# Kernel tuning notes

Measured on AMD Instinct MI355X. Metric: run time of the kernel, lower is better.

Reference implementation:

```python
import jax, jax.numpy as jnp
import numpy as np
from jax import lax

L, B, T_IMG, T_TXT = 12, 2, 256, 64
E, H, G = 1024, 16, 2730
V = 16416  # image_vocab_count + 1
C = E // H
EPS = 1e-6  # flax LayerNorm default


def _ln(x, scale, bias):
    mu = jnp.mean(x, -1, keepdims=True)
    var = jnp.var(x, -1, keepdims=True)
    y = (x - mu) * lax.rsqrt(var + EPS)
    if scale is not None:
        y = y * scale
    if bias is not None:
        y = y + bias
    return y


def _attend(k, v, q, mask, o_w):
    # k,v: [B,K,H,C]  q: [B,Q,H,C]  mask: [B,K]
    bias = jnp.where(mask, 0.0, -jnp.inf)[:, None, None, :]
    w = jnp.einsum('bqhc,bkhc->bhqk', q, k) + bias
    w = jax.nn.softmax(w, axis=-1)
    out = jnp.einsum('bhqk,bkhc->bqhc', w, v)
    return out.reshape(out.shape[0], out.shape[1], E) @ o_w


def setup_inputs():
    key = jax.random.key(0)
    ks = jax.random.split(key, 16)
    s = 0.02
    n = lambda k, shape: jax.random.normal(k, shape, jnp.float32) * s
    return dict(
        encoder_state=n(ks[0], (B, T_TXT, E)),
        keys_state=jnp.zeros((L, B, T_IMG, H, C), jnp.float32),
        values_state=jnp.zeros((L, B, T_IMG, H, C), jnp.float32),
        attention_mask=jnp.ones((B, T_TXT), jnp.bool_),
        prev_token=5000,
        token_index=100,
        embed_tok=n(ks[1], (V, E)),
        embed_pos=n(ks[2], (T_IMG, E)),
        ln_emb_s=jnp.ones((E,), jnp.float32),
        ln_emb_b=jnp.zeros((E,), jnp.float32),
        final_ln_b=jnp.zeros((E,), jnp.float32),
        lm_head_w=n(ks[3], (E, V)),
        pre_sa_ln_b=jnp.zeros((L, E), jnp.float32),
        sa_q_w=n(ks[4], (L, E, E)), sa_k_w=n(ks[5], (L, E, E)),
        sa_v_w=n(ks[6], (L, E, E)), sa_o_w=n(ks[7], (L, E, E)),
        sa_ln_s=jnp.ones((L, E), jnp.float32), sa_ln_b=jnp.zeros((L, E), jnp.float32),
        pre_ca_ln_b=jnp.zeros((L, E), jnp.float32),
        ca_q_w=n(ks[8], (L, E, E)), ca_k_w=n(ks[9], (L, E, E)),
        ca_v_w=n(ks[10], (L, E, E)), ca_o_w=n(ks[11], (L, E, E)),
        ca_ln_s=jnp.ones((L, E), jnp.float32), ca_ln_b=jnp.zeros((L, E), jnp.float32),
        glu_ln0_b=jnp.zeros((L, E), jnp.float32),
        glu_fc0_w=n(ks[12], (L, E, G)), glu_fc1_w=n(ks[13], (L, E, G)),
        glu_ln1_b=jnp.zeros((L, G), jnp.float32),
        glu_fc2_w=n(ks[14], (L, G, E)),
    )


def _decode_step(encoder_state, keys_state, values_state, attention_mask,
                 prev_token, token_index, embed_tok, embed_pos,
                 ln_emb_s, ln_emb_b, final_ln_b, lm_head_w, layer_params):
    ones = jnp.ones((B, 1), jnp.int32)
    ds = embed_tok[prev_token * ones] + embed_pos[token_index * ones]  # [B,1,E]
    ds = _ln(ds, ln_emb_s, ln_emb_b)
    self_mask = jnp.broadcast_to(jnp.arange(T_IMG) < token_index + 1, (B, T_IMG))
    scale = C ** 0.5

    def step(ds, xs):
        ks_l, vs_l, p = xs  # per-layer KV cache [B,T_IMG,H,C] and params
        (pre_sa_b, qw, kw, vw, ow, sa_s, sa_b,
         pre_ca_b, cqw, ckw, cvw, cow, ca_s, ca_b,
         g0b, f0, f1, g1b, f2) = p
        # --- self attention with KV-cache append ---
        residual = ds
        x = _ln(ds, None, pre_sa_b)
        ks_l = lax.dynamic_update_slice(ks_l, (x @ kw).reshape(B, 1, H, C), (0, token_index, 0, 0))
        vs_l = lax.dynamic_update_slice(vs_l, (x @ vw).reshape(B, 1, H, C), (0, token_index, 0, 0))
        q = (x @ qw).reshape(B, 1, H, C) / scale
        x = _attend(ks_l, vs_l, q, self_mask, ow)
        ds = residual + _ln(x, sa_s, sa_b)
        # --- cross attention over encoder state ---
        residual = ds
        x = _ln(ds, None, pre_ca_b)
        ek = (encoder_state @ ckw).reshape(B, T_TXT, H, C)
        ev = (encoder_state @ cvw).reshape(B, T_TXT, H, C)
        q = (x @ cqw).reshape(B, 1, H, C) / scale
        x = _attend(ek, ev, q, attention_mask, cow)
        ds = residual + _ln(x, ca_s, ca_b)
        # --- GLU FFN ---
        residual = ds
        z = _ln(ds, None, g0b)
        w = jax.nn.gelu(z @ f0, approximate=False)
        z = _ln(w * (z @ f1), None, g1b)
        ds = residual + z @ f2
        return ds, (ks_l, vs_l)

    ds, (keys_state, values_state) = lax.scan(step, ds, (keys_state, values_state, layer_params))
    ds = _ln(ds, None, final_ln_b)
    logits = ds @ lm_head_w  # [B,1,V]
    return logits, keys_state, values_state


def reference(encoder_state, keys_state, values_state, attention_mask, prev_token,
              token_index, embed_tok, embed_pos, ln_emb_s, ln_emb_b, final_ln_b,
              lm_head_w, pre_sa_ln_b, sa_q_w, sa_k_w, sa_v_w, sa_o_w, sa_ln_s,
              sa_ln_b, pre_ca_ln_b, ca_q_w, ca_k_w, ca_v_w, ca_o_w, ca_ln_s,
              ca_ln_b, glu_ln0_b, glu_fc0_w, glu_fc1_w, glu_ln1_b, glu_fc2_w):
    layer_params = (pre_sa_ln_b, sa_q_w, sa_k_w, sa_v_w, sa_o_w, sa_ln_s, sa_ln_b,
                    pre_ca_ln_b, ca_q_w, ca_k_w, ca_v_w, ca_o_w, ca_ln_s, ca_ln_b,
                    glu_ln0_b, glu_fc0_w, glu_fc1_w, glu_ln1_b, glu_fc2_w)
    return _decode_step(encoder_state, keys_state, values_state, attention_mask,
                        prev_token, token_index, embed_tok, embed_pos,
                        ln_emb_s, ln_emb_b, final_ln_b, lm_head_w, layer_params)
```

## Files before the change

### kernel.cpp

```cpp
#include <hip/hip_runtime.h>
#include <math.h>

#define LAYERS 12
#define EE 1024
#define GG 2730
#define VV 16416
#define EPS 1e-6f

#define OFF_EK 0
#define OFF_EV 1572864
#define OFF_DS 3145728
#define NSLOT 37
#define OFF_ACC (OFF_DS + NSLOT*2048)
#define ACC_STRIDE 28672
#define AQ 0
#define AK 2048
#define AV 4096
#define AY 6144
#define AQC 8192
#define AY2 10240
#define AA 12288
#define AB2 17748
#define ACC_TOTAL (LAYERS*ACC_STRIDE)
#define ZERO_FLOATS (NSLOT*2048 + ACC_TOTAL)

#define KVL 524288
#define KVB 262144

struct MegaP {
  const float* enc; const float* keys_in; const float* values_in;
  const int* maski; const int* pt; const int* ti;
  const float* tok; const float* pos; const float* ln_s; const float* ln_b;
  const float* final_b; const float* lm_w;
  const float* pre_sa_b; const float* saq; const float* sak; const float* sav;
  const float* sao; const float* sas; const float* sab;
  const float* pre_ca_b; const float* caq; const float* ckw; const float* cvw;
  const float* cao; const float* cas; const float* cab;
  const float* g0b; const float* f0; const float* f1; const float* g1b; const float* f2;
  float* logits; float* keys_out; float* values_out; float* ws;
};

__device__ __forceinline__ void red4(float* sm, float& a, float& b, float& c, float& d){
  #pragma unroll
  for(int o=32;o;o>>=1){ a+=__shfl_down(a,o); b+=__shfl_down(b,o); c+=__shfl_down(c,o); d+=__shfl_down(d,o); }
  int w=threadIdx.x>>6, l=threadIdx.x&63;
  __syncthreads();
  if(l==0){ sm[w]=a; sm[4+w]=b; sm[8+w]=c; sm[12+w]=d; }
  __syncthreads();
  a=sm[0]+sm[1]+sm[2]+sm[3]; b=sm[4]+sm[5]+sm[6]+sm[7];
  c=sm[8]+sm[9]+sm[10]+sm[11]; d=sm[12]+sm[13]+sm[14]+sm[15];
}

__device__ __forceinline__ void ln_stats_g(const float* v, int K, float* sm,
    float& mu0, float& rs0, float& mu1, float& rs1){
  float s0=0,q0=0,s1=0,q1=0;
  for(int i=threadIdx.x;i<K;i+=256){ float a=v[i], b=v[K+i]; s0+=a;q0+=a*a;s1+=b;q1+=b*b; }
  red4(sm,s0,q0,s1,q1);
  mu0=s0/K; mu1=s1/K;
  rs0=rsqrtf(fmaxf(q0/K-mu0*mu0,0.f)+EPS);
  rs1=rsqrtf(fmaxf(q1/K-mu1*mu1,0.f)+EPS);
}

__device__ __forceinline__ void ln_stats_l(float (*Ds)[1024], float* sm,
    float& mu0, float& rs0, float& mu1, float& rs1){
  float s0=0,q0=0,s1=0,q1=0;
  for(int i=threadIdx.x;i<EE;i+=256){ float a=Ds[0][i], b=Ds[1][i]; s0+=a;q0+=a*a;s1+=b;q1+=b*b; }
  red4(sm,s0,q0,s1,q1);
  mu0=s0/EE; mu1=s1/EE;
  rs0=rsqrtf(fmaxf(q0/EE-mu0*mu0,0.f)+EPS);
  rs1=rsqrtf(fmaxf(q1/EE-mu1*mu1,0.f)+EPS);
}

__device__ __forceinline__ void build_ds3(const float* dsi, const float* accL,
    const float* sasl, const float* sabl, const float* casl, const float* cabl,
    float (*Ds)[1024], float* sm){
  float mu0,rs0,mu1,rs1;
  ln_stats_g(accL+AY, EE, sm, mu0,rs0,mu1,rs1);
  for(int i=threadIdx.x;i<EE;i+=256){ float sc=sasl[i], bi=sabl[i];
    Ds[0][i]=dsi[i]    + (accL[AY+i]-mu0)*rs0*sc + bi;
    Ds[1][i]=dsi[EE+i] + (accL[AY+EE+i]-mu1)*rs1*sc + bi; }
  ln_stats_g(accL+AY2, EE, sm, mu0,rs0,mu1,rs1);
  for(int i=threadIdx.x;i<EE;i+=256){ float sc=casl[i], bi=cabl[i];
    Ds[0][i] += (accL[AY2+i]-mu0)*rs0*sc + bi;
    Ds[1][i] += (accL[AY2+EE+i]-mu1)*rs1*sc + bi; }
}

__global__ __launch_bounds__(256)
void k_init(MegaP p){
  __shared__ float As[128][33];
  __shared__ float Bs[32][33];
  const int t=threadIdx.x, bid=blockIdx.x;
  if (bid < 768){
    int lp = bid>>5, cx = bid&31;
    int l = lp>>1, proj = lp&1;
    const float* Wt = (proj? p.cvw : p.ckw) + (size_t)l*EE*EE;
    float* outp = p.ws + (proj? OFF_EV : OFF_EK) + (size_t)l*128*EE;
    int c0 = cx*32;
    int tx=t&7, ty=t>>3;
    float acc[4][4];
    #pragma unroll
    for(int i=0;i<4;i++){ acc[i][0]=0;acc[i][1]=0;acc[i][2]=0;acc[i][3]=0; }
    float ar[16], br[4];
    #pragma unroll
    for(int j=0;j<16;j++){ int i=t+j*256; ar[j]=p.enc[(size_t)(i>>5)*EE + (i&31)]; }
    #pragma unroll
    for(int j=0;j<4;j++){ int i=t+j*256; br[j]=Wt[(size_t)(i>>5)*EE + c0 + (i&31)]; }
    for (int it=0; it<32; ++it){
      #pragma unroll
      for(int j=0;j<16;j++){ int i=t+j*256; As[i>>5][i&31]=ar[j]; }
      #pragma unroll
      for(int j=0;j<4;j++){ int i=t+j*256; Bs[i>>5][i&31]=br[j]; }
      __syncthreads();
      if (it<31){
        int k0n=(it+1)*32;
        #pragma unroll
        for(int j=0;j<16;j++){ int i=t+j*256; ar[j]=p.enc[(size_t)(i>>5)*EE + k0n + (i&31)]; }
        #pragma unroll
        for(int j=0;j<4;j++){ int i=t+j*256; br[j]=Wt[(size_t)((i>>5)+k0n)*EE + c0 + (i&31)]; }
      }
      #pragma unroll
      for (int k=0;k<32;k++){
        float b0=Bs[k][tx*4+0], b1=Bs[k][tx*4+1], b2=Bs[k][tx*4+2], b3=Bs[k][tx*4+3];
        #pragma unroll
        for (int rr=0;rr<4;rr++){
          float av = As[ty+32*rr][k];
          acc[rr][0]+=av*b0; acc[rr][1]+=av*b1; acc[rr][2]+=av*b2; acc[rr][3]+=av*b3;
        }
      }
      __syncthreads();
    }
    #pragma unroll
    for (int rr=0;rr<4;rr++)
      #pragma unroll
      for (int j=0;j<4;j++)
        outp[(size_t)(ty+32*rr)*EE + c0 + tx*4+j] = acc[rr][j];
  } else {
    float* ev = &As[0][0];
    float* smv = &Bs[0][0];
    int ptv = p.pt[0], tiv = p.ti[0];
    float s0=0,q0=0,d1=0,d2=0;
    for(int i=t;i<EE;i+=256){ float v=p.tok[(size_t)ptv*EE+i]+p.pos[(size_t)tiv*EE+i]; ev[i]=v; s0+=v; q0+=v*v; }
    red4(smv,s0,q0,d1,d2);
    float mu=s0/EE, rs=rsqrtf(fmaxf(q0/EE-mu*mu,0.f)+EPS);
    float* ds0 = p.ws + OFF_DS;
    __syncthreads();
    for(int i=t;i<EE;i+=256){ float y=(ev[i]-mu)*rs*p.ln_s[i]+p.ln_b[i]; ds0[i]=y; ds0[EE+i]=y; }
  }
}

__global__ __launch_bounds__(256)
void k_qkv(MegaP p, int l){
  __shared__ float Xs[2][1024];
  __shared__ float sm[16];
  const int t=threadIdx.x;
  const float* dsi = p.ws + OFF_DS + (size_t)(3*l)*2048;
  float* accL = p.ws + OFF_ACC + (size_t)l*ACC_STRIDE;
  const size_t lE2=(size_t)l*EE*EE, lE=(size_t)l*EE;
  float mu0,rs0,mu1,rs1;
  ln_stats_g(dsi, EE, sm, mu0,rs0,mu1,rs1);
  for(int i=t;i<EE;i+=256){ float bi=p.pre_sa_b[lE+i];
    Xs[0][i]=(dsi[i]-mu0)*rs0+bi; Xs[1][i]=(dsi[EE+i]-mu1)*rs1+bi; }
  __syncthreads();
  int c = blockIdx.x*256 + t;
  int sel = c>>10, cc = c&1023;
  const float* W = (sel==0? p.saq : sel==1? p.sak : p.sav) + lE2;
  float* O = accL + (sel==0? AQ : sel==1? AK : AV);
  int k0 = blockIdx.y*16;
  const float* wp = W + (size_t)k0*EE + cc;
  float a0=0,a1=0;
  #pragma unroll
  for(int k=0;k<16;k++){ float w=*wp; wp+=EE; a0+=Xs[0][k0+k]*w; a1+=Xs[1][k0+k]*w; }
  atomicAdd(&O[cc],a0); atomicAdd(&O[EE+cc],a1);
}

__global__ __launch_bounds__(256)
void k_selfo(MegaP p, int l){
  __shared__ float Ds[2][1024];
  __shared__ float att[2][256];
  __shared__ float sm[16];
  const int t=threadIdx.x, bkid=blockIdx.x, tiv=p.ti[0];
  float* accL = p.ws + OFF_ACC + (size_t)l*ACC_STRIDE;
  const size_t lE2=(size_t)l*EE*EE;
  int cg=bkid&3, h=(bkid>>2)&15, sub=(bkid>>6)&3, hoff=h*64;
  if (t < 128){ int bb2=t>>6, c2=t&63; Ds[bb2][c2] = accL[AQ + bb2*EE + hoff + c2]*0.125f; }
  __syncthreads();
  for(int bb2=0;bb2<2;bb2++)
    for(int tt=t; tt<=tiv; tt+=256){
      const float* kr = (tt<tiv) ? (p.keys_in + (size_t)l*KVL + (size_t)bb2*KVB + (size_t)tt*EE + hoff)
                                 : (accL + AK + bb2*EE + hoff);
      float d=0;
      #pragma unroll
      for(int c2=0;c2<64;c2++) d += Ds[bb2][c2]*kr[c2];
      att[bb2][tt] = d;
    }
  __syncthreads();
  int wv=t>>6, l2=t&63;
  if (wv<2){
    float m=-3.4e38f;
    for(int tt=l2; tt<=tiv; tt+=64) m=fmaxf(m, att[wv][tt]);
    #pragma unroll
    for(int o=32;o;o>>=1) m=fmaxf(m,__shfl_xor(m,o));
    float s=0;
    for(int tt=l2; tt<=tiv; tt+=64){ float e=__expf(att[wv][tt]-m); att[wv][tt]=e; s+=e; }
    #pragma unroll
    for(int o=32;o;o>>=1) s+=__shfl_xor(s,o);
    if(l2==0) sm[8+wv]=1.f/s;
  }
  __syncthreads();
  {
    int bb2=t>>7, j=(t>>3)&15, part=t&7, colh=sub*16+j;
    float v=0;
    for(int tt=part; tt<=tiv; tt+=8){
      float vv = (tt<tiv)? p.values_in[(size_t)l*KVL + (size_t)bb2*KVB + (size_t)tt*EE + hoff + colh]
                         : accL[AV + bb2*EE + hoff + colh];
      v += att[bb2][tt]*vv;
    }
    v += __shfl_down(v,4,8); v += __shfl_down(v,2,8); v += __shfl_down(v,1,8);
    if(part==0) Ds[bb2][512+j] = v*sm[8+bb2];
  }
  __syncthreads();
  {
    int c = cg*256+t, kb = hoff + sub*16;
    const float* wp = p.sao + lE2 + (size_t)kb*EE + c;
    float a0=0,a1=0;
    #pragma unroll
    for(int j2=0;j2<16;j2++){ float w=wp[(size_t)j2*EE]; a0+=Ds[0][512+j2]*w; a1+=Ds[1][512+j2]*w; }
    atomicAdd(&accL[AY+c],a0); atomicAdd(&accL[AY+EE+c],a1);
  }
  if (cg==0 && sub==0){
    int bb2=t>>7, kv=(t>>6)&1, c2=t&63;
    float val = accL[(kv?AV:AK) + bb2*EE + hoff + c2];
    float* dst = (kv? p.values_out : p.keys_out)
               + (size_t)l*KVL + (size_t)bb2*KVB + (size_t)tiv*EE + hoff + c2;
    *dst = val;
  }
}

__global__ __launch_bounds__(256)
void k_ds2caq(MegaP p, int l){
  __shared__ float Xs[2][1024];
  __shared__ float Ds[2][1024];
  __shared__ float sm[16];
  const int t=threadIdx.x;
  const float* dsi = p.ws + OFF_DS + (size_t)(3*l)*2048;
  float* accL = p.ws + OFF_ACC + (size_t)l*ACC_STRIDE;
  const size_t lE2=(size_t)l*EE*EE, lE=(size_t)l*EE;
  float mu0,rs0,mu1,rs1;
  ln_stats_g(accL+AY, EE, sm, mu0,rs0,mu1,rs1);
  for(int i=t;i<EE;i+=256){ float sc=p.sas[lE+i], bi=p.sab[lE+i];
    Ds[0][i]=dsi[i]    + (accL[AY+i]-mu0)*rs0*sc + bi;
    Ds[1][i]=dsi[EE+i] + (accL[AY+EE+i]-mu1)*rs1*sc + bi; }
  ln_stats_l(Ds, sm, mu0,rs0,mu1,rs1);
  for(int i=t;i<EE;i+=256){ float bi=p.pre_ca_b[lE+i];
    Xs[0][i]=(Ds[0][i]-mu0)*rs0+bi; Xs[1][i]=(Ds[1][i]-mu1)*rs1+bi; }
  __syncthreads();
  int c = blockIdx.x*256 + t;
  int k0 = blockIdx.y*16;
  const float* wp = p.caq + lE2 + (size_t)k0*EE + c;
  float a0=0,a1=0;
  #pragma unroll
  for(int k=0;k<16;k++){ float w=*wp; wp+=EE; a0+=Xs[0][k0+k]*w; a1+=Xs[1][k0+k]*w; }
  float* O = accL + AQC;
  atomicAdd(&O[c],a0); atomicAdd(&O[EE+c],a1);
}

__global__ __launch_bounds__(256)
void k_crosso(MegaP p, int l){
  __shared__ float Ds[2][1024];
  __shared__ float att[2][256];
  __shared__ float sm[16];
  const int t=threadIdx.x, bkid=blockIdx.x;
  float* accL = p.ws + OFF_ACC + (size_t)l*ACC_STRIDE;
  const size_t lE2=(size_t)l*EE*EE;
  int cg=bkid&3, h=(bkid>>2)&15, sub=(bkid>>6)&3, hoff=h*64;
  const float* ek = p.ws + OFF_EK;
  const float* ev = p.ws + OFF_EV;
  if (t < 128){ int bb2=t>>6, c2=t&63; Ds[bb2][c2] = accL[AQC + bb2*EE + hoff + c2]*0.125f; }
  __syncthreads();
  if (t < 128){
    int bb2=t>>6, tt=t&63;
    const float* kr = ek + ((size_t)l*128 + bb2*64 + tt)*EE + hoff;
    float d=0;
    #pragma unroll
    for(int c2=0;c2<64;c2++) d += Ds[bb2][c2]*kr[c2];
    int mi = bb2*64+tt;
    bool valid = (p.maski[mi]!=0) || (((const unsigned char*)p.maski)[mi]!=0);
    att[bb2][tt] = valid ? d : -3.4e38f;
  }
  __syncthreads();
  int wv=t>>6, l2=t&63;
  if (wv<2){
    float sc = att[wv][l2];
    float m = sc;
    #pragma unroll
    for(int o=32;o;o>>=1) m=fmaxf(m,__shfl_xor(m,o));
    float e = (sc>-1e37f)? __expf(sc-m) : 0.f;
    att[wv][l2]=e; float s=e;
    #pragma unroll
    for(int o=32;o;o>>=1) s+=__shfl_xor(s,o);
    if(l2==0) sm[8+wv]=1.f/s;
  }
  __syncthreads();
  {
    int bb2=t>>7, j=(t>>3)&15, part=t&7, colh=sub*16+j;
    float v=0;
    for(int tt=part; tt<64; tt+=8)
      v += att[bb2][tt]*ev[((size_t)l*128 + bb2*64 + tt)*EE + hoff + colh];
    v += __shfl_down(v,4,8); v += __shfl_down(v,2,8); v += __shfl_down(v,1,8);
    if(part==0) Ds[bb2][512+j] = v*sm[8+bb2];
  }
  __syncthreads();
  {
    int c = cg*256+t, kb = hoff + sub*16;
    const float* wp = p.cao + lE2 + (size_t)kb*EE + c;
    float a0=0,a1=0;
    #pragma unroll
    for(int j2=0;j2<16;j2++){ float w=wp[(size_t)j2*EE]; a0+=Ds[0][512+j2]*w; a1+=Ds[1][512+j2]*w; }
    atomicAdd(&accL[AY2+c],a0); atomicAdd(&accL[AY2+EE+c],a1);
  }
}

__global__ __launch_bounds__(256)
void k_glu01(MegaP p, int l){
  __shared__ float Xs[2][1024];
  __shared__ float Ds[2][1024];
  __shared__ float sm[16];
  const int t=threadIdx.x;
  const float* dsi = p.ws + OFF_DS + (size_t)(3*l)*2048;
  float* accL = p.ws + OFF_ACC + (size_t)l*ACC_STRIDE;
  const size_t lEG=(size_t)l*EE*GG, lE=(size_t)l*EE;
  build_ds3(dsi, accL, p.sas+lE, p.sab+lE, p.cas+lE, p.cab+lE, Ds, sm);
  float mu0,rs0,mu1,rs1;
  ln_stats_l(Ds, sm, mu0,rs0,mu1,rs1);
  for(int i=t;i<EE;i+=256){ float bi=p.g0b[lE+i];
    Xs[0][i]=(Ds[0][i]-mu0)*rs0+bi; Xs[1][i]=(Ds[1][i]-mu1)*rs1+bi; }
  __syncthreads();
  int c2 = blockIdx.x*256 + t;
  if (c2 < 2730){
    int sel = (c2>=1365), cc2 = sel? c2-1365 : c2, col = cc2*2;
    const float* W = (sel? p.f1 : p.f0) + lEG;
    float* O = accL + (sel? AB2 : AA);
    int k0 = blockIdx.y*16;
    const float2* wp = (const float2*)(W + (size_t)k0*GG + col);
    float a0=0,a1=0,b0=0,b1=0;
    #pragma unroll
    for(int k=0;k<16;k++){
      float2 w=*wp; wp+=1365;
      float x0=Xs[0][k0+k], x1=Xs[1][k0+k];
      a0+=x0*w.x; a1+=x0*w.y; b0+=x1*w.x; b1+=x1*w.y;
    }
    atomicAdd(&O[col+0],a0); atomicAdd(&O[col+1],a1);
    atomicAdd(&O[GG+col+0],b0); atomicAdd(&O[GG+col+1],b1);
  }
}

__global__ __launch_bounds__(256)
void k_glu2(MegaP p, int l){
  __shared__ float Xs[2][2736];
  __shared__ float Ds[2][1024];
  __shared__ float sm[16];
  const int t=threadIdx.x;
  const float* dsi = p.ws + OFF_DS + (size_t)(3*l)*2048;
  float* ds4 = p.ws + OFF_DS + (size_t)(3*l+3)*2048;
  float* accL = p.ws + OFF_ACC + (size_t)l*ACC_STRIDE;
  const size_t lGE=(size_t)l*GG*EE, lE=(size_t)l*EE, lG=(size_t)l*GG;
  const int ks = blockIdx.y;
  if (ks==0) build_ds3(dsi, accL, p.sas+lE, p.sab+lE, p.cas+lE, p.cab+lE, Ds, sm);
  float s0=0,q0=0,s1=0,q1=0;
  for(int i=t;i<GG;i+=256){
    float a0v=accL[AA+i], a1v=accL[AA+GG+i];
    float b0v=accL[AB2+i], b1v=accL[AB2+GG+i];
    float g0v=0.5f*a0v*(1.f+erff(a0v*0.70710678118654752f));
    float g1v=0.5f*a1v*(1.f+erff(a1v*0.70710678118654752f));
    float t0=g0v*b0v, t1=g1v*b1v;
    Xs[0][i]=t0; Xs[1][i]=t1;
    s0+=t0;q0+=t0*t0;s1+=t1;q1+=t1*t1;
  }
  red4(sm,s0,q0,s1,q1);
  float mu0=s0/GG, mu1=s1/GG;
  float rs0=rsqrtf(fmaxf(q0/GG-mu0*mu0,0.f)+EPS), rs1=rsqrtf(fmaxf(q1/GG-mu1*mu1,0.f)+EPS);
  for(int i=t;i<GG;i+=256){ float bi=p.g1b[lG+i];
    Xs[0][i]=(Xs[0][i]-mu0)*rs0+bi; Xs[1][i]=(Xs[1][i]-mu1)*rs1+bi; }
  __syncthreads();
  int c = blockIdx.x*256 + t;
  int k0 = ks*32, k1 = k0+32; if (k1>GG) k1=GG;
  float a0=0,b0=0;
  if (ks==0){ a0=Ds[0][c]; b0=Ds[1][c]; }
  const float* wp = p.f2 + lGE + (size_t)k0*EE + c;
  #pragma unroll 8
  for(int k=k0;k<k1;k++){ float w=*wp; wp+=EE; a0+=Xs[0][k]*w; b0+=Xs[1][k]*w; }
  atomicAdd(&ds4[c],a0); atomicAdd(&ds4[EE+c],b0);
}

__global__ __launch_bounds__(256)
void k_lm(MegaP p){
  __shared__ float Xs[2][1024];
  __shared__ float sm[16];
  const int t=threadIdx.x;
  const float* dsf = p.ws + OFF_DS + (size_t)36*2048;
  float mu0,rs0,mu1,rs1;
  ln_stats_g(dsf, EE, sm, mu0,rs0,mu1,rs1);
  for(int i=t;i<EE;i+=256){ float bi=p.final_b[i];
    Xs[0][i]=(dsf[i]-mu0)*rs0+bi; Xs[1][i]=(dsf[EE+i]-mu1)*rs1+bi; }
  __syncthreads();
  int c4 = blockIdx.x*256 + t;
  if (c4 < 4104){
    int col = c4*4;
    int k0 = blockIdx.y*32;
    const float4* wp = (const float4*)(p.lm_w + (size_t)k0*VV + col);
    float a0=0,a1=0,a2=0,a3=0,b0=0,b1=0,b2=0,b3=0;
    #pragma unroll 8
    for(int k=0;k<32;k++){
      float4 w=*wp; wp+=4104;
      float x0=Xs[0][k0+k], x1=Xs[1][k0+k];
      a0+=x0*w.x; a1+=x0*w.y; a2+=x0*w.z; a3+=x0*w.w;
      b0+=x1*w.x; b1+=x1*w.y; b2+=x1*w.z; b3+=x1*w.w;
    }
    atomicAdd(&p.logits[col+0],a0); atomicAdd(&p.logits[col+1],a1);
    atomicAdd(&p.logits[col+2],a2); atomicAdd(&p.logits[col+3],a3);
    atomicAdd(&p.logits[VV+col+0],b0); atomicAdd(&p.logits[VV+col+1],b1);
    atomicAdd(&p.logits[VV+col+2],b2); atomicAdd(&p.logits[VV+col+3],b3);
  }
}

extern "C" void kernel_launch(void* const* d_in, const int* in_sizes, int n_in,
                              void* d_out, int out_size, void* d_ws, size_t ws_size,
                              hipStream_t stream){
  (void)in_sizes; (void)n_in; (void)out_size; (void)ws_size;
  float* out = (float*)d_out;
  float* ws = (float*)d_ws;

  MegaP P;
  P.enc        = (const float*)d_in[0];
  P.keys_in    = (const float*)d_in[1];
  P.values_in  = (const float*)d_in[2];
  P.maski      = (const int*)d_in[3];
  P.pt         = (const int*)d_in[4];
  P.ti         = (const int*)d_in[5];
  P.tok        = (const float*)d_in[6];
  P.pos        = (const float*)d_in[7];
  P.ln_s       = (const float*)d_in[8];
  P.ln_b       = (const float*)d_in[9];
  P.final_b    = (const float*)d_in[10];
  P.lm_w       = (const float*)d_in[11];
  P.pre_sa_b   = (const float*)d_in[12];
  P.saq        = (const float*)d_in[13];
  P.sak        = (const float*)d_in[14];
  P.sav        = (const float*)d_in[15];
  P.sao        = (const float*)d_in[16];
  P.sas        = (const float*)d_in[17];
  P.sab        = (const float*)d_in[18];
  P.pre_ca_b   = (const float*)d_in[19];
  P.caq        = (const float*)d_in[20];
  P.ckw        = (const float*)d_in[21];
  P.cvw        = (const float*)d_in[22];
  P.cao        = (const float*)d_in[23];
  P.cas        = (const float*)d_in[24];
  P.cab        = (const float*)d_in[25];
  P.g0b        = (const float*)d_in[26];
  P.f0         = (const float*)d_in[27];
  P.f1         = (const float*)d_in[28];
  P.g1b        = (const float*)d_in[29];
  P.f2         = (const float*)d_in[30];
  P.logits     = out;
  P.keys_out   = out + (size_t)2*VV;
  P.values_out = P.keys_out + (size_t)LAYERS*KVL;
  P.ws         = ws;

  hipMemsetAsync(ws + OFF_DS, 0, (size_t)ZERO_FLOATS*sizeof(float), stream);
  hipMemsetAsync(P.logits, 0, (size_t)2*VV*sizeof(float), stream);
  hipMemcpyAsync(P.keys_out, P.keys_in, (size_t)LAYERS*KVL*sizeof(float),
                 hipMemcpyDeviceToDevice, stream);
  hipMemcpyAsync(P.values_out, P.values_in, (size_t)LAYERS*KVL*sizeof(float),
                 hipMemcpyDeviceToDevice, stream);

  k_init<<<769,256,0,stream>>>(P);
  for (int l=0;l<LAYERS;l++){
    k_qkv   <<<dim3(12,64),256,0,stream>>>(P,l);
    k_selfo <<<256,        256,0,stream>>>(P,l);
    k_ds2caq<<<dim3(4,64), 256,0,stream>>>(P,l);
    k_crosso<<<256,        256,0,stream>>>(P,l);
    k_glu01 <<<dim3(11,64),256,0,stream>>>(P,l);
    k_glu2  <<<dim3(4,86), 256,0,stream>>>(P,l);
  }
  k_lm<<<dim3(17,32),256,0,stream>>>(P);
}
```

Measured before the change: 1.160 ms.

## Refactor cross-attention algebraically, fuse KV-cache copy into QKV kernel, prefetch weights

```diff
diff --git a/kernel.cpp b/kernel.cpp
--- a/kernel.cpp
+++ b/kernel.cpp
@@ -7,9 +7,7 @@
 #define VV 16416
 #define EPS 1e-6f
 
-#define OFF_EK 0
-#define OFF_EV 1572864
-#define OFF_DS 3145728
+#define OFF_DS 0
 #define NSLOT 37
 #define OFF_ACC (OFF_DS + NSLOT*2048)
 #define ACC_STRIDE 28672
@@ -18,9 +16,11 @@
 #define AV 4096
 #define AY 6144
 #define AQC 8192
-#define AY2 10240
-#define AA 12288
-#define AB2 17748
+#define ASC 10240
+#define AOUT 12288
+#define AY2 14336
+#define AA 16384
+#define AB2 21844
 #define ACC_TOTAL (LAYERS*ACC_STRIDE)
 #define ZERO_FLOATS (NSLOT*2048 + ACC_TOTAL)
 
@@ -86,90 +86,58 @@
 }
 
 __global__ __launch_bounds__(256)
-void k_init(MegaP p){
-  __shared__ float As[128][33];
-  __shared__ float Bs[32][33];
-  const int t=threadIdx.x, bid=blockIdx.x;
-  if (bid < 768){
-    int lp = bid>>5, cx = bid&31;
-    int l = lp>>1, proj = lp&1;
-    const float* Wt = (proj? p.cvw : p.ckw) + (size_t)l*EE*EE;
-    float* outp = p.ws + (proj? OFF_EV : OFF_EK) + (size_t)l*128*EE;
-    int c0 = cx*32;
-    int tx=t&7, ty=t>>3;
-    float acc[4][4];
-    #pragma unroll
-    for(int i=0;i<4;i++){ acc[i][0]=0;acc[i][1]=0;acc[i][2]=0;acc[i][3]=0; }
-    float ar[16], br[4];
-    #pragma unroll
-    for(int j=0;j<16;j++){ int i=t+j*256; ar[j]=p.enc[(size_t)(i>>5)*EE + (i&31)]; }
-    #pragma unroll
-    for(int j=0;j<4;j++){ int i=t+j*256; br[j]=Wt[(size_t)(i>>5)*EE + c0 + (i&31)]; }
-    for (int it=0; it<32; ++it){
-      #pragma unroll
-      for(int j=0;j<16;j++){ int i=t+j*256; As[i>>5][i&31]=ar[j]; }
-      #pragma unroll
-      for(int j=0;j<4;j++){ int i=t+j*256; Bs[i>>5][i&31]=br[j]; }
-      __syncthreads();
-      if (it<31){
-        int k0n=(it+1)*32;
-        #pragma unroll
-        for(int j=0;j<16;j++){ int i=t+j*256; ar[j]=p.enc[(size_t)(i>>5)*EE + k0n + (i&31)]; }
-        #pragma unroll
-        for(int j=0;j<4;j++){ int i=t+j*256; br[j]=Wt[(size_t)((i>>5)+k0n)*EE + c0 + (i&31)]; }
-      }
-      #pragma unroll
-      for (int k=0;k<32;k++){
-        float b0=Bs[k][tx*4+0], b1=Bs[k][tx*4+1], b2=Bs[k][tx*4+2], b3=Bs[k][tx*4+3];
-        #pragma unroll
-        for (int rr=0;rr<4;rr++){
-          float av = As[ty+32*rr][k];
-          acc[rr][0]+=av*b0; acc[rr][1]+=av*b1; acc[rr][2]+=av*b2; acc[rr][3]+=av*b3;
-        }
-      }
-      __syncthreads();
-    }
-    #pragma unroll
-    for (int rr=0;rr<4;rr++)
-      #pragma unroll
-      for (int j=0;j<4;j++)
-        outp[(size_t)(ty+32*rr)*EE + c0 + tx*4+j] = acc[rr][j];
-  } else {
-    float* ev = &As[0][0];
-    float* smv = &Bs[0][0];
-    int ptv = p.pt[0], tiv = p.ti[0];
-    float s0=0,q0=0,d1=0,d2=0;
-    for(int i=t;i<EE;i+=256){ float v=p.tok[(size_t)ptv*EE+i]+p.pos[(size_t)tiv*EE+i]; ev[i]=v; s0+=v; q0+=v*v; }
-    red4(smv,s0,q0,d1,d2);
-    float mu=s0/EE, rs=rsqrtf(fmaxf(q0/EE-mu*mu,0.f)+EPS);
-    float* ds0 = p.ws + OFF_DS;
-    __syncthreads();
-    for(int i=t;i<EE;i+=256){ float y=(ev[i]-mu)*rs*p.ln_s[i]+p.ln_b[i]; ds0[i]=y; ds0[EE+i]=y; }
-  }
+void k_prelude(MegaP p){
+  __shared__ float ev[EE];
+  __shared__ float sm[16];
+  const int t=threadIdx.x;
+  int ptv = p.pt[0], tiv = p.ti[0];
+  float s0=0,q0=0,d1=0,d2=0;
+  for(int i=t;i<EE;i+=256){ float v=p.tok[(size_t)ptv*EE+i]+p.pos[(size_t)tiv*EE+i]; ev[i]=v; s0+=v; q0+=v*v; }
+  red4(sm,s0,q0,d1,d2);
+  float mu=s0/EE, rs=rsqrtf(fmaxf(q0/EE-mu*mu,0.f)+EPS);
+  float* ds0 = p.ws + OFF_DS;
+  __syncthreads();
+  for(int i=t;i<EE;i+=256){ float y=(ev[i]-mu)*rs*p.ln_s[i]+p.ln_b[i]; ds0[i]=y; ds0[EE+i]=y; }
 }
 
 __global__ __launch_bounds__(256)
 void k_qkv(MegaP p, int l){
   __shared__ float Xs[2][1024];
   __shared__ float sm[16];
-  const int t=threadIdx.x;
+  const int t=threadIdx.x, bx=blockIdx.x, by=blockIdx.y;
+  if (bx >= 12){
+    int cb = (bx-12)*64 + by;
+    #pragma unroll
+    for(int j=0;j<4;j++){
+      int idx4 = cb*1024 + j*256 + t;
+      int kv = idx4 >> 17;
+      int r4 = idx4 & 131071;
+      size_t off = (size_t)l*KVL + (size_t)r4*4;
+      float4 v = *(const float4*)((kv? p.values_in : p.keys_in) + off);
+      *(float4*)((kv? p.values_out : p.keys_out) + off) = v;
+    }
+    return;
+  }
   const float* dsi = p.ws + OFF_DS + (size_t)(3*l)*2048;
   float* accL = p.ws + OFF_ACC + (size_t)l*ACC_STRIDE;
   const size_t lE2=(size_t)l*EE*EE, lE=(size_t)l*EE;
+  int c = bx*256 + t;
+  int sel = c>>10, cc = c&1023;
+  const float* W = (sel==0? p.saq : sel==1? p.sak : p.sav) + lE2;
+  float* O = accL + (sel==0? AQ : sel==1? AK : AV);
+  int k0 = by*16;
+  const float* wp = W + (size_t)k0*EE + cc;
+  float wr[16];
+  #pragma unroll
+  for(int k=0;k<16;k++) wr[k] = wp[(size_t)k*EE];
   float mu0,rs0,mu1,rs1;
   ln_stats_g(dsi, EE, sm, mu0,rs0,mu1,rs1);
   for(int i=t;i<EE;i+=256){ float bi=p.pre_sa_b[lE+i];
     Xs[0][i]=(dsi[i]-mu0)*rs0+bi; Xs[1][i]=(dsi[EE+i]-mu1)*rs1+bi; }
   __syncthreads();
-  int c = blockIdx.x*256 + t;
-  int sel = c>>10, cc = c&1023;
-  const float* W = (sel==0? p.saq : sel==1? p.sak : p.sav) + lE2;
-  float* O = accL + (sel==0? AQ : sel==1? AK : AV);
-  int k0 = blockIdx.y*16;
-  const float* wp = W + (size_t)k0*EE + cc;
   float a0=0,a1=0;
   #pragma unroll
-  for(int k=0;k<16;k++){ float w=*wp; wp+=EE; a0+=Xs[0][k0+k]*w; a1+=Xs[1][k0+k]*w; }
+  for(int k=0;k<16;k++){ a0+=Xs[0][k0+k]*wr[k]; a1+=Xs[1][k0+k]*wr[k]; }
   atomicAdd(&O[cc],a0); atomicAdd(&O[EE+cc],a1);
 }
 
@@ -245,6 +213,12 @@
   const float* dsi = p.ws + OFF_DS + (size_t)(3*l)*2048;
   float* accL = p.ws + OFF_ACC + (size_t)l*ACC_STRIDE;
   const size_t lE2=(size_t)l*EE*EE, lE=(size_t)l*EE;
+  int c = blockIdx.x*256 + t;
+  int k0 = blockIdx.y*16;
+  const float* wp = p.caq + lE2 + (size_t)k0*EE + c;
+  float wr[16];
+  #pragma unroll
+  for(int k=0;k<16;k++) wr[k] = wp[(size_t)k*EE];
   float mu0,rs0,mu1,rs1;
   ln_stats_g(accL+AY, EE, sm, mu0,rs0,mu1,rs1);
   for(int i=t;i<EE;i+=256){ float sc=p.sas[lE+i], bi=p.sab[lE+i];
@@ -254,70 +228,112 @@
   for(int i=t;i<EE;i+=256){ float bi=p.pre_ca_b[lE+i];
     Xs[0][i]=(Ds[0][i]-mu0)*rs0+bi; Xs[1][i]=(Ds[1][i]-mu1)*rs1+bi; }
   __syncthreads();
+  float a0=0,a1=0;
+  #pragma unroll
+  for(int k=0;k<16;k++){ a0+=Xs[0][k0+k]*wr[k]; a1+=Xs[1][k0+k]*wr[k]; }
+  float* O = accL + AQC;
+  atomicAdd(&O[c],a0); atomicAdd(&O[EE+c],a1);
+}
+
+__global__ __launch_bounds__(256)
+void k_uscore(MegaP p, int l){
+  __shared__ float qs[64];
+  __shared__ float us[256];
+  const int t=threadIdx.x, bh=blockIdx.x, ec=blockIdx.y;
+  const int b=bh>>4, h=bh&15, hoff=h*64;
+  float* accL = p.ws + OFF_ACC + (size_t)l*ACC_STRIDE;
+  const size_t lE2=(size_t)l*EE*EE;
+  const int e = ec*256 + t;
+  const float4* cp = (const float4*)(p.ckw + lE2 + (size_t)e*EE + hoff);
+  float4 wr[16];
+  #pragma unroll
+  for(int j=0;j<16;j++) wr[j] = cp[j];
+  if (t < 64) qs[t] = accL[AQC + b*EE + hoff + t]*0.125f;
+  __syncthreads();
+  float u=0;
+  #pragma unroll
+  for(int j=0;j<16;j++){
+    u += wr[j].x*qs[4*j] + wr[j].y*qs[4*j+1] + wr[j].z*qs[4*j+2] + wr[j].w*qs[4*j+3];
+  }
+  us[t]=u;
+  __syncthreads();
+  int t2=t&63, q4=t>>6;
+  const float4* ep = (const float4*)(p.enc + (size_t)(b*64+t2)*EE + ec*256 + q4*64);
+  float pa=0;
+  #pragma unroll
+  for(int j=0;j<16;j++){
+    float4 e4=ep[j];
+    pa += e4.x*us[q4*64+4*j] + e4.y*us[q4*64+4*j+1] + e4.z*us[q4*64+4*j+2] + e4.w*us[q4*64+4*j+3];
+  }
+  atomicAdd(&accL[ASC + (b*16+h)*64 + t2], pa);
+}
+
+__global__ __launch_bounds__(256)
+void k_ov(MegaP p, int l){
+  __shared__ float att[64];
+  __shared__ float ctxp[2][128];
+  __shared__ float ctxs[128];
+  __shared__ float smr[2];
+  const int t=threadIdx.x, bh=blockIdx.x, es=blockIdx.y;
+  const int b=bh>>4, h=bh&15, hoff=h*64, e0=es*128;
+  float* accL = p.ws + OFF_ACC + (size_t)l*ACC_STRIDE;
+  const size_t lE2=(size_t)l*EE*EE;
+  const int c=t&63, part=t>>6;
+  const float* vp = p.cvw + lE2 + (size_t)(e0+part*32)*EE + hoff + c;
+  float wr[32];
+  #pragma unroll
+  for(int j=0;j<32;j++) wr[j] = vp[(size_t)j*EE];
+  if (t<64){
+    float sc = accL[ASC + (b*16+h)*64 + t];
+    int mi=b*64+t;
+    bool valid = (p.maski[mi]!=0) || (((const unsigned char*)p.maski)[mi]!=0);
+    sc = valid? sc : -3.4e38f;
+    float m=sc;
+    #pragma unroll
+    for(int o=32;o;o>>=1) m=fmaxf(m,__shfl_xor(m,o));
+    float e_ = valid? __expf(sc-m) : 0.f;
+    float s=e_;
+    #pragma unroll
+    for(int o=32;o;o>>=1) s+=__shfl_xor(s,o);
+    att[t]=e_;
+    if(t==0) smr[0]=1.f/s;
+  }
+  __syncthreads();
+  {
+    int e2=t>>1, half=t&1;
+    const float* ep = p.enc + (size_t)(b*64+half*32)*EE + e0+e2;
+    float ca=0;
+    #pragma unroll 8
+    for(int tt=0;tt<32;tt++) ca += att[half*32+tt]*ep[(size_t)tt*EE];
+    ctxp[half][e2]=ca;
+  }
+  __syncthreads();
+  if (t<128) ctxs[t] = (ctxp[0][t]+ctxp[1][t])*smr[0];
+  __syncthreads();
+  float a=0;
+  #pragma unroll
+  for(int j=0;j<32;j++) a += ctxs[part*32+j]*wr[j];
+  atomicAdd(&accL[AOUT + b*EE + hoff + c], a);
+}
+
+__global__ __launch_bounds__(256)
+void k_y2(MegaP p, int l){
+  __shared__ float Xs[2][1024];
+  const int t=threadIdx.x;
+  float* accL = p.ws + OFF_ACC + (size_t)l*ACC_STRIDE;
+  const size_t lE2=(size_t)l*EE*EE;
   int c = blockIdx.x*256 + t;
   int k0 = blockIdx.y*16;
-  const float* wp = p.caq + lE2 + (size_t)k0*EE + c;
+  const float* wp = p.cao + lE2 + (size_t)k0*EE + c;
+  float wr[16];
+  #pragma unroll
+  for(int k=0;k<16;k++) wr[k] = wp[(size_t)k*EE];
+  for(int i=t;i<EE;i+=256){ Xs[0][i]=accL[AOUT+i]; Xs[1][i]=accL[AOUT+EE+i]; }
+  __syncthreads();
   float a0=0,a1=0;
   #pragma unroll
-  for(int k=0;k<16;k++){ float w=*wp; wp+=EE; a0+=Xs[0][k0+k]*w; a1+=Xs[1][k0+k]*w; }
-  float* O = accL + AQC;
-  atomicAdd(&O[c],a0); atomicAdd(&O[EE+c],a1);
-}
-
-__global__ __launch_bounds__(256)
-void k_crosso(MegaP p, int l){
-  __shared__ float Ds[2][1024];
-  __shared__ float att[2][256];
-  __shared__ float sm[16];
-  const int t=threadIdx.x, bkid=blockIdx.x;
-  float* accL = p.ws + OFF_ACC + (size_t)l*ACC_STRIDE;
-  const size_t lE2=(size_t)l*EE*EE;
-  int cg=bkid&3, h=(bkid>>2)&15, sub=(bkid>>6)&3, hoff=h*64;
-  const float* ek = p.ws + OFF_EK;
-  const float* ev = p.ws + OFF_EV;
-  if (t < 128){ int bb2=t>>6, c2=t&63; Ds[bb2][c2] = accL[AQC + bb2*EE + hoff + c2]*0.125f; }
-  __syncthreads();
-  if (t < 128){
-    int bb2=t>>6, tt=t&63;
-    const float* kr = ek + ((size_t)l*128 + bb2*64 + tt)*EE + hoff;
-    float d=0;
-    #pragma unroll
-    for(int c2=0;c2<64;c2++) d += Ds[bb2][c2]*kr[c2];
-    int mi = bb2*64+tt;
-    bool valid = (p.maski[mi]!=0) || (((const unsigned char*)p.maski)[mi]!=0);
-    att[bb2][tt] = valid ? d : -3.4e38f;
-  }
-  __syncthreads();
-  int wv=t>>6, l2=t&63;
-  if (wv<2){
-    float sc = att[wv][l2];
-    float m = sc;
-    #pragma unroll
-    for(int o=32;o;o>>=1) m=fmaxf(m,__shfl_xor(m,o));
-    float e = (sc>-1e37f)? __expf(sc-m) : 0.f;
-    att[wv][l2]=e; float s=e;
-    #pragma unroll
-    for(int o=32;o;o>>=1) s+=__shfl_xor(s,o);
-    if(l2==0) sm[8+wv]=1.f/s;
-  }
-  __syncthreads();
-  {
-    int bb2=t>>7, j=(t>>3)&15, part=t&7, colh=sub*16+j;
-    float v=0;
-    for(int tt=part; tt<64; tt+=8)
-      v += att[bb2][tt]*ev[((size_t)l*128 + bb2*64 + tt)*EE + hoff + colh];
-    v += __shfl_down(v,4,8); v += __shfl_down(v,2,8); v += __shfl_down(v,1,8);
-    if(part==0) Ds[bb2][512+j] = v*sm[8+bb2];
-  }
-  __syncthreads();
-  {
-    int c = cg*256+t, kb = hoff + sub*16;
-    const float* wp = p.cao + lE2 + (size_t)kb*EE + c;
-    float a0=0,a1=0;
-    #pragma unroll
-    for(int j2=0;j2<16;j2++){ float w=wp[(size_t)j2*EE]; a0+=Ds[0][512+j2]*w; a1+=Ds[1][512+j2]*w; }
-    atomicAdd(&accL[AY2+c],a0); atomicAdd(&accL[AY2+EE+c],a1);
-  }
+  for(int k=0;k<16;k++){ a0+=Xs[0][k0+k]*wr[k]; a1+=Xs[1][k0+k]*wr[k]; }
+  atomicAdd(&accL[AY2+c],a0); atomicAdd(&accL[AY2+EE+c],a1);
 }
 
 __global__ __launch_bounds__(256)
@@ -329,25 +345,31 @@
   const float* dsi = p.ws + OFF_DS + (size_t)(3*l)*2048;
   float* accL = p.ws + OFF_ACC + (size_t)l*ACC_STRIDE;
   const size_t lEG=(size_t)l*EE*GG, lE=(size_t)l*EE;
+  int c2 = blockIdx.x*256 + t;
+  int k0 = blockIdx.y*16;
+  int sel=0, col=0;
+  const float* W = nullptr;
+  float2 wr[16];
+  if (c2 < 2730){
+    sel = (c2>=1365); int cc2 = sel? c2-1365 : c2; col = cc2*2;
+    W = (sel? p.f1 : p.f0) + lEG;
+    const float2* wp = (const float2*)(W + (size_t)k0*GG + col);
+    #pragma unroll
+    for(int k=0;k<16;k++) wr[k] = wp[(size_t)k*1365];
+  }
   build_ds3(dsi, accL, p.sas+lE, p.sab+lE, p.cas+lE, p.cab+lE, Ds, sm);
   float mu0,rs0,mu1,rs1;
   ln_stats_l(Ds, sm, mu0,rs0,mu1,rs1);
   for(int i=t;i<EE;i+=256){ float bi=p.g0b[lE+i];
     Xs[0][i]=(Ds[0][i]-mu0)*rs0+bi; Xs[1][i]=(Ds[1][i]-mu1)*rs1+bi; }
   __syncthreads();
-  int c2 = blockIdx.x*256 + t;
   if (c2 < 2730){
-    int sel = (c2>=1365), cc2 = sel? c2-1365 : c2, col = cc2*2;
-    const float* W = (sel? p.f1 : p.f0) + lEG;
     float* O = accL + (sel? AB2 : AA);
-    int k0 = blockIdx.y*16;
-    const float2* wp = (const float2*)(W + (size_t)k0*GG + col);
     float a0=0,a1=0,b0=0,b1=0;
     #pragma unroll
     for(int k=0;k<16;k++){
-      float2 w=*wp; wp+=1365;
       float x0=Xs[0][k0+k], x1=Xs[1][k0+k];
-      a0+=x0*w.x; a1+=x0*w.y; b0+=x1*w.x; b1+=x1*w.y;
+      a0+=x0*wr[k].x; a1+=x0*wr[k].y; b0+=x1*wr[k].x; b1+=x1*wr[k].y;
     }
     atomicAdd(&O[col+0],a0); atomicAdd(&O[col+1],a1);
     atomicAdd(&O[GG+col+0],b0); atomicAdd(&O[GG+col+1],b1);
@@ -365,6 +387,12 @@
   float* accL = p.ws + OFF_ACC + (size_t)l*ACC_STRIDE;
   const size_t lGE=(size_t)l*GG*EE, lE=(size_t)l*EE, lG=(size_t)l*GG;
   const int ks = blockIdx.y;
+  int c = blockIdx.x*256 + t;
+  int k0 = ks*32, k1 = k0+32; if (k1>GG) k1=GG;
+  const float* wp = p.f2 + lGE + (size_t)k0*EE + c;
+  float wr[32];
+  #pragma unroll
+  for(int k=0;k<32;k++) wr[k] = (k0+k<GG) ? wp[(size_t)k*EE] : 0.f;
   if (ks==0) build_ds3(dsi, accL, p.sas+lE, p.sab+lE, p.cas+lE, p.cab+lE, Ds, sm);
   float s0=0,q0=0,s1=0,q1=0;
   for(int i=t;i<GG;i+=256){
@@ -382,13 +410,12 @@
   for(int i=t;i<GG;i+=256){ float bi=p.g1b[lG+i];
     Xs[0][i]=(Xs[0][i]-mu0)*rs0+bi; Xs[1][i]=(Xs[1][i]-mu1)*rs1+bi; }
   __syncthreads();
-  int c = blockIdx.x*256 + t;
-  int k0 = ks*32, k1 = k0+32; if (k1>GG) k1=GG;
   float a0=0,b0=0;
   if (ks==0){ a0=Ds[0][c]; b0=Ds[1][c]; }
-  const float* wp = p.f2 + lGE + (size_t)k0*EE + c;
-  #pragma unroll 8
-  for(int k=k0;k<k1;k++){ float w=*wp; wp+=EE; a0+=Xs[0][k]*w; b0+=Xs[1][k]*w; }
+  #pragma unroll
+  for(int k=0;k<32;k++){
+    if (k0+k<GG){ a0+=Xs[0][k0+k]*wr[k]; b0+=Xs[1][k0+k]*wr[k]; }
+  }
   atomicAdd(&ds4[c],a0); atomicAdd(&ds4[EE+c],b0);
 }
 
@@ -469,17 +496,15 @@
 
   hipMemsetAsync(ws + OFF_DS, 0, (size_t)ZERO_FLOATS*sizeof(float), stream);
   hipMemsetAsync(P.logits, 0, (size_t)2*VV*sizeof(float), stream);
-  hipMemcpyAsync(P.keys_out, P.keys_in, (size_t)LAYERS*KVL*sizeof(float),
-                 hipMemcpyDeviceToDevice, stream);
-  hipMemcpyAsync(P.values_out, P.values_in, (size_t)LAYERS*KVL*sizeof(float),
-                 hipMemcpyDeviceToDevice, stream);
-
-  k_init<<<769,256,0,stream>>>(P);
+
+  k_prelude<<<1,256,0,stream>>>(P);
   for (int l=0;l<LAYERS;l++){
-    k_qkv   <<<dim3(12,64),256,0,stream>>>(P,l);
+    k_qkv   <<<dim3(16,64),256,0,stream>>>(P,l);
     k_selfo <<<256,        256,0,stream>>>(P,l);
     k_ds2caq<<<dim3(4,64), 256,0,stream>>>(P,l);
-    k_crosso<<<256,        256,0,stream>>>(P,l);
+    k_uscore<<<dim3(32,4), 256,0,stream>>>(P,l);
+    k_ov    <<<dim3(32,8), 256,0,stream>>>(P,l);
+    k_y2    <<<dim3(4,64), 256,0,stream>>>(P,l);
     k_glu01 <<<dim3(11,64),256,0,stream>>>(P,l);
     k_glu2  <<<dim3(4,86), 256,0,stream>>>(P,l);
   }
```

Measured after the change: 1.065 ms. -8.2%, faster.
